# Performance work log

Measured on AMD Instinct MI355X. Metric: run time of the kernel, lower is better.

Reference implementation:

```python
import jax, jax.numpy as jnp
import numpy as np

U = 200000      # unique nodes
B = 20000       # node_list batch size
K = 33          # n_nbr_samples + self
F = 256         # feature_dim
E = 128         # emb_dim
BN_EPS = 1e-5


def setup_inputs() -> dict:
    key = jax.random.key(0)
    k1, k2, k3, k4 = jax.random.split(key, 4)
    return {
        "features": jax.random.normal(k1, (U, F), dtype=jnp.float32),
        "W": jax.random.normal(k2, (F, E), dtype=jnp.float32) * 0.05,
        "b": jax.random.normal(k3, (E,), dtype=jnp.float32) * 0.01,
        "gamma": jnp.ones((E,), dtype=jnp.float32),
        "beta": jnp.zeros((E,), dtype=jnp.float32),
        "sample_idx": jax.random.randint(k4, (B, K), 0, U, dtype=jnp.int64)
        if jax.config.jax_enable_x64 else jax.random.randint(k4, (B, K), 0, U, dtype=jnp.int32),
    }


def reference(features, W, b, gamma, beta, sample_idx):
    # fc: Linear -> BatchNorm1d (training-mode batch stats) -> Tanh; Dropout in eval (identity)
    h = features @ W + b                       # [U, E]
    mu = jnp.mean(h, axis=0)                   # [E]
    var = jnp.var(h, axis=0)                   # biased var, as torch BN uses for normalization
    h = jnp.tanh(gamma * (h - mu) * jax.lax.rsqrt(var + BN_EPS) + beta)  # [U, E]
    # Row-normalized 0/1 mask matmul == mean over the K distinct sampled unique-node rows
    gathered = h[sample_idx]                   # [B, K, E] irregular gather
    return jnp.mean(gathered, axis=1)          # [B, E]
```

## Files before the change

kernel.cpp:

```cpp
#include <hip/hip_runtime.h>

#define U_NODES 200000
#define B_ROWS  20000
#define K_S     33
#define F_DIM   256
#define E_DIM   128

typedef __bf16 bf16x8 __attribute__((ext_vector_type(8)));
typedef float  f32x4  __attribute__((ext_vector_type(4)));
typedef unsigned short ushortx4 __attribute__((ext_vector_type(4)));
typedef unsigned short ushortx8 __attribute__((ext_vector_type(8)));

__device__ __forceinline__ unsigned short f2bf(float f) {
    unsigned int u = __builtin_bit_cast(unsigned int, f);
    u += 0x7fffu + ((u >> 16) & 1u);
    return (unsigned short)(u >> 16);
}
__device__ __forceinline__ float bf2f(unsigned short s) {
    return __builtin_bit_cast(float, ((unsigned int)s) << 16);
}

__global__ void wprep_kernel(const float* __restrict__ W, unsigned short* __restrict__ Wt) {
    int n = blockIdx.x;
    int k = threadIdx.x;
    Wt[n * F_DIM + k] = f2bf(W[(size_t)k * E_DIM + n]);
}

__global__ __launch_bounds__(256) void gemm_stats_kernel(
    const float* __restrict__ A, const unsigned short* __restrict__ Wt,
    unsigned short* __restrict__ h, float* __restrict__ gsum, float* __restrict__ gsq)
{
    __shared__ __attribute__((aligned(16))) char smem[32768];
    char* As = smem;
    char* Ws = smem + 16384;

    const int t    = threadIdx.x;
    const int lane = t & 63;
    const int wv   = t >> 6;
    const int m    = lane & 15;
    const int qd   = lane >> 4;
    const int row0 = blockIdx.x * 128;

    f32x4 acc0[8], acc1[8];
    #pragma unroll
    for (int ct = 0; ct < 8; ++ct) {
        acc0[ct] = (f32x4){0.f, 0.f, 0.f, 0.f};
        acc1[ct] = (f32x4){0.f, 0.f, 0.f, 0.f};
    }

    for (int kk = 0; kk < F_DIM; kk += 64) {
        #pragma unroll
        for (int i = 0; i < 8; ++i) {
            int flat = t + 256 * i;
            int r  = flat >> 4;
            int c4 = (flat & 15) * 4;
            int gr = row0 + r; if (gr >= U_NODES) gr = U_NODES - 1;
            float4 v = *(const float4*)(A + (size_t)gr * F_DIM + kk + c4);
            int q = c4 >> 3, half = (c4 >> 2) & 1;
            ushortx4 w4 = { f2bf(v.x), f2bf(v.y), f2bf(v.z), f2bf(v.w) };
            *(ushortx4*)(As + r * 128 + ((q ^ (r & 7)) << 4) + half * 8) = w4;
        }
        #pragma unroll
        for (int i = 0; i < 4; ++i) {
            int flat = t + 256 * i;
            int r = flat >> 3, q = flat & 7;
            ushortx8 v = *(const ushortx8*)(Wt + (size_t)r * F_DIM + kk + q * 8);
            *(ushortx8*)(Ws + r * 128 + ((q ^ (r & 7)) << 4)) = v;
        }
        __syncthreads();
        #pragma unroll
        for (int ks = 0; ks < 2; ++ks) {
            int q = ks * 4 + qd;
            int r0 = wv * 32 + m;
            int r1 = r0 + 16;
            bf16x8 a0 = *(const bf16x8*)(As + r0 * 128 + ((q ^ (r0 & 7)) << 4));
            bf16x8 a1 = *(const bf16x8*)(As + r1 * 128 + ((q ^ (r1 & 7)) << 4));
            #pragma unroll
            for (int ct = 0; ct < 8; ++ct) {
                int rb = ct * 16 + m;
                bf16x8 b = *(const bf16x8*)(Ws + rb * 128 + ((q ^ (rb & 7)) << 4));
                acc0[ct] = __builtin_amdgcn_mfma_f32_16x16x32_bf16(a0, b, acc0[ct], 0, 0, 0);
                acc1[ct] = __builtin_amdgcn_mfma_f32_16x16x32_bf16(a1, b, acc1[ct], 0, 0, 0);
            }
        }
        __syncthreads();
    }

    const bool full = (row0 + 128) <= U_NODES;
    float s[8], sq[8];
    #pragma unroll
    for (int ct = 0; ct < 8; ++ct) {
        float ss = 0.f, qq = 0.f;
        #pragma unroll
        for (int v = 0; v < 4; ++v) {
            float x0 = acc0[ct][v];
            float x1 = acc1[ct][v];
            if (full || (row0 + wv * 32 + qd * 4 + v) < U_NODES)      { ss += x0; qq += x0 * x0; }
            if (full || (row0 + wv * 32 + 16 + qd * 4 + v) < U_NODES) { ss += x1; qq += x1 * x1; }
        }
        s[ct] = ss; sq[ct] = qq;
    }
    float* red = (float*)smem;
    int rq = wv * 4 + qd;
    #pragma unroll
    for (int ct = 0; ct < 8; ++ct) red[rq * 128 + ct * 16 + m] = s[ct];
    __syncthreads();
    if (t < 128) {
        float tot = 0.f;
        #pragma unroll
        for (int i = 0; i < 16; ++i) tot += red[i * 128 + t];
        atomicAdd(&gsum[t], tot);
    }
    __syncthreads();
    #pragma unroll
    for (int ct = 0; ct < 8; ++ct) red[rq * 128 + ct * 16 + m] = sq[ct];
    __syncthreads();
    if (t < 128) {
        float tot = 0.f;
        #pragma unroll
        for (int i = 0; i < 16; ++i) tot += red[i * 128 + t];
        atomicAdd(&gsq[t], tot);
    }
    __syncthreads();

    unsigned short* tb = (unsigned short*)(smem + wv * 8192);
    #pragma unroll
    for (int ct = 0; ct < 8; ++ct)
        #pragma unroll
        for (int v = 0; v < 4; ++v) {
            tb[(qd * 4 + v) * 128 + ct * 16 + m]        = f2bf(acc0[ct][v]);
            tb[(16 + qd * 4 + v) * 128 + ct * 16 + m]   = f2bf(acc1[ct][v]);
        }
    __syncthreads();
    #pragma unroll
    for (int i = 0; i < 8; ++i) {
        int idx = lane + 64 * i;
        int r = idx >> 4, c8 = (idx & 15) * 8;
        int gr = row0 + wv * 32 + r;
        if (gr < U_NODES)
            *(ushortx8*)(h + (size_t)gr * E_DIM + c8) = *(const ushortx8*)(tb + r * 128 + c8);
    }
}

__global__ void finalize_kernel(const float* __restrict__ gsum, const float* __restrict__ gsq,
                                const float* __restrict__ gamma, const float* __restrict__ beta,
                                float* __restrict__ scale, float* __restrict__ shift)
{
    int e = threadIdx.x;
    float mu  = gsum[e] * (1.f / U_NODES);
    float var = gsq[e] * (1.f / U_NODES) - mu * mu;
    float inv = rsqrtf(var + 1e-5f);
    float sc  = gamma[e] * inv;
    scale[e] = sc;
    shift[e] = beta[e] - sc * mu;
}

__global__ __launch_bounds__(256) void gather_kernel(
    const unsigned short* __restrict__ h, const int* __restrict__ sidx_g,
    const float* __restrict__ scale, const float* __restrict__ shift,
    float* __restrict__ out)
{
    __shared__ int sl[16 * K_S];
    const int t  = threadIdx.x;
    const int g  = t & 15;
    const int r  = t >> 4;
    const int b0 = blockIdx.x * 16;
    for (int i = t; i < 16 * K_S; i += 256) sl[i] = sidx_g[(size_t)b0 * K_S + i];
    float scv[8], shv[8];
    *(float4*)&scv[0] = *(const float4*)(scale + g * 8);
    *(float4*)&scv[4] = *(const float4*)(scale + g * 8 + 4);
    *(float4*)&shv[0] = *(const float4*)(shift + g * 8);
    *(float4*)&shv[4] = *(const float4*)(shift + g * 8 + 4);
    __syncthreads();

    float acc[8] = {0.f, 0.f, 0.f, 0.f, 0.f, 0.f, 0.f, 0.f};
    #pragma unroll
    for (int k = 0; k < K_S; ++k) {
        int idx = sl[r * K_S + k];
        ushortx8 v = *(const ushortx8*)(h + (size_t)idx * E_DIM + g * 8);
        #pragma unroll
        for (int j = 0; j < 8; ++j) {
            float x  = bf2f(v[j]) * scv[j] + shv[j];
            float ex = __expf(2.f * x);
            acc[j] += 1.f - 2.f * __builtin_amdgcn_rcpf(ex + 1.f);
        }
    }
    float* op = out + (size_t)(b0 + r) * E_DIM + g * 8;
    *(float4*)(op)     = make_float4(acc[0] * (1.f / K_S), acc[1] * (1.f / K_S),
                                     acc[2] * (1.f / K_S), acc[3] * (1.f / K_S));
    *(float4*)(op + 4) = make_float4(acc[4] * (1.f / K_S), acc[5] * (1.f / K_S),
                                     acc[6] * (1.f / K_S), acc[7] * (1.f / K_S));
}

extern "C" void kernel_launch(void* const* d_in, const int* in_sizes, int n_in,
                              void* d_out, int out_size, void* d_ws, size_t ws_size,
                              hipStream_t stream) {
    const float* features = (const float*)d_in[0];
    const float* W        = (const float*)d_in[1];
    const float* gamma    = (const float*)d_in[3];
    const float* beta     = (const float*)d_in[4];
    const int*   sample   = (const int*)d_in[5];
    float* out = (float*)d_out;

    float* gsum  = (float*)d_ws;
    float* gsq   = gsum + 128;
    float* scale = gsq + 128;
    float* shift = scale + 128;
    unsigned short* Wt = (unsigned short*)(shift + 128);
    unsigned short* h  = Wt + 128 * 256;

    hipMemsetAsync(gsum, 0, 2 * 128 * sizeof(float), stream);
    wprep_kernel<<<128, 256, 0, stream>>>(W, Wt);
    gemm_stats_kernel<<<(U_NODES + 127) / 128, 256, 0, stream>>>(features, Wt, h, gsum, gsq);
    finalize_kernel<<<1, 128, 0, stream>>>(gsum, gsq, gamma, beta, scale, shift);
    gather_kernel<<<B_ROWS / 16, 256, 0, stream>>>(h, sample, scale, shift, out);
}
```

Baseline: 343.4 us.

## Load A fragments directly to registers with double-buffered prefetch; stage full W once

The GEMM no longer stages the feature tile through LDS. Each lane loads its own A fragment from global memory into registers, converts it to bf16 in registers, and double-buffers the loads so the next K-chunk is fetched while MFMAs run on the current one. All of W (256x128 bf16) is staged into LDS once, which removes the per-chunk barriers, and the sum and sum-of-squares reductions now share one pass. The cost is a 64KB LDS allocation, which may limit occupancy, plus more registers and less coalesced global reads of A.

```diff
diff --git a/kernel.cpp b/kernel.cpp
--- a/kernel.cpp
+++ b/kernel.cpp
@@ -19,6 +19,12 @@
 __device__ __forceinline__ float bf2f(unsigned short s) {
     return __builtin_bit_cast(float, ((unsigned int)s) << 16);
 }
+__device__ __forceinline__ bf16x8 pack_bf8(f32x4 a, f32x4 b) {
+    ushortx8 r;
+    r[0] = f2bf(a[0]); r[1] = f2bf(a[1]); r[2] = f2bf(a[2]); r[3] = f2bf(a[3]);
+    r[4] = f2bf(b[0]); r[5] = f2bf(b[1]); r[6] = f2bf(b[2]); r[7] = f2bf(b[3]);
+    return __builtin_bit_cast(bf16x8, r);
+}
 
 __global__ void wprep_kernel(const float* __restrict__ W, unsigned short* __restrict__ Wt) {
     int n = blockIdx.x;
@@ -30,9 +36,8 @@
     const float* __restrict__ A, const unsigned short* __restrict__ Wt,
     unsigned short* __restrict__ h, float* __restrict__ gsum, float* __restrict__ gsq)
 {
-    __shared__ __attribute__((aligned(16))) char smem[32768];
-    char* As = smem;
-    char* Ws = smem + 16384;
+    __shared__ __attribute__((aligned(16))) char smem[65536];
+    char* Ws = smem;
 
     const int t    = threadIdx.x;
     const int lane = t & 63;
@@ -41,6 +46,52 @@
     const int qd   = lane >> 4;
     const int row0 = blockIdx.x * 128;
 
+    int gr0 = row0 + wv * 32 + m;       if (gr0 >= U_NODES) gr0 = U_NODES - 1;
+    int gr1 = row0 + wv * 32 + 16 + m;  if (gr1 >= U_NODES) gr1 = U_NODES - 1;
+    const float* pa0 = A + (size_t)gr0 * F_DIM + qd * 8;
+    const float* pa1 = A + (size_t)gr1 * F_DIM + qd * 8;
+
+#define LOAD_CHUNK(P, c) do {                                                  \
+        P[0] = *(const f32x4*)(pa0 + (c) * 64);                                \
+        P[1] = *(const f32x4*)(pa0 + (c) * 64 + 4);                            \
+        P[2] = *(const f32x4*)(pa0 + (c) * 64 + 32);                           \
+        P[3] = *(const f32x4*)(pa0 + (c) * 64 + 36);                           \
+        P[4] = *(const f32x4*)(pa1 + (c) * 64);                                \
+        P[5] = *(const f32x4*)(pa1 + (c) * 64 + 4);                            \
+        P[6] = *(const f32x4*)(pa1 + (c) * 64 + 32);                           \
+        P[7] = *(const f32x4*)(pa1 + (c) * 64 + 36);                           \
+    } while (0)
+
+#define COMPUTE_CHUNK(P, c) do {                                               \
+        bf16x8 a00 = pack_bf8(P[0], P[1]);                                     \
+        bf16x8 a01 = pack_bf8(P[2], P[3]);                                     \
+        bf16x8 a10 = pack_bf8(P[4], P[5]);                                     \
+        bf16x8 a11 = pack_bf8(P[6], P[7]);                                     \
+        _Pragma("unroll")                                                      \
+        for (int ct = 0; ct < 8; ++ct) {                                       \
+            int rb = ct * 16 + m;                                              \
+            bf16x8 b0 = *(const bf16x8*)(Ws + rb * 512 +                       \
+                            ((((c) * 8 + qd) ^ (rb & 7)) << 4));               \
+            acc0[ct] = __builtin_amdgcn_mfma_f32_16x16x32_bf16(a00, b0, acc0[ct], 0, 0, 0); \
+            acc1[ct] = __builtin_amdgcn_mfma_f32_16x16x32_bf16(a10, b0, acc1[ct], 0, 0, 0); \
+            bf16x8 b1 = *(const bf16x8*)(Ws + rb * 512 +                       \
+                            ((((c) * 8 + 4 + qd) ^ (rb & 7)) << 4));           \
+            acc0[ct] = __builtin_amdgcn_mfma_f32_16x16x32_bf16(a01, b1, acc0[ct], 0, 0, 0); \
+            acc1[ct] = __builtin_amdgcn_mfma_f32_16x16x32_bf16(a11, b1, acc1[ct], 0, 0, 0); \
+        }                                                                      \
+    } while (0)
+
+    f32x4 p0[8], p1[8];
+    LOAD_CHUNK(p0, 0);
+
+    #pragma unroll
+    for (int i = 0; i < 16; ++i) {
+        int flat = t + 256 * i;
+        int r = flat >> 5, q = flat & 31;
+        ushortx8 v = *(const ushortx8*)(Wt + (size_t)r * F_DIM + q * 8);
+        *(ushortx8*)(Ws + r * 512 + ((q ^ (r & 7)) << 4)) = v;
+    }
+
     f32x4 acc0[8], acc1[8];
     #pragma unroll
     for (int ct = 0; ct < 8; ++ct) {
@@ -48,43 +99,20 @@
         acc1[ct] = (f32x4){0.f, 0.f, 0.f, 0.f};
     }
 
-    for (int kk = 0; kk < F_DIM; kk += 64) {
-        #pragma unroll
-        for (int i = 0; i < 8; ++i) {
-            int flat = t + 256 * i;
-            int r  = flat >> 4;
-            int c4 = (flat & 15) * 4;
-            int gr = row0 + r; if (gr >= U_NODES) gr = U_NODES - 1;
-            float4 v = *(const float4*)(A + (size_t)gr * F_DIM + kk + c4);
-            int q = c4 >> 3, half = (c4 >> 2) & 1;
-            ushortx4 w4 = { f2bf(v.x), f2bf(v.y), f2bf(v.z), f2bf(v.w) };
-            *(ushortx4*)(As + r * 128 + ((q ^ (r & 7)) << 4) + half * 8) = w4;
-        }
-        #pragma unroll
-        for (int i = 0; i < 4; ++i) {
-            int flat = t + 256 * i;
-            int r = flat >> 3, q = flat & 7;
-            ushortx8 v = *(const ushortx8*)(Wt + (size_t)r * F_DIM + kk + q * 8);
-            *(ushortx8*)(Ws + r * 128 + ((q ^ (r & 7)) << 4)) = v;
-        }
-        __syncthreads();
-        #pragma unroll
-        for (int ks = 0; ks < 2; ++ks) {
-            int q = ks * 4 + qd;
-            int r0 = wv * 32 + m;
-            int r1 = r0 + 16;
-            bf16x8 a0 = *(const bf16x8*)(As + r0 * 128 + ((q ^ (r0 & 7)) << 4));
-            bf16x8 a1 = *(const bf16x8*)(As + r1 * 128 + ((q ^ (r1 & 7)) << 4));
-            #pragma unroll
-            for (int ct = 0; ct < 8; ++ct) {
-                int rb = ct * 16 + m;
-                bf16x8 b = *(const bf16x8*)(Ws + rb * 128 + ((q ^ (rb & 7)) << 4));
-                acc0[ct] = __builtin_amdgcn_mfma_f32_16x16x32_bf16(a0, b, acc0[ct], 0, 0, 0);
-                acc1[ct] = __builtin_amdgcn_mfma_f32_16x16x32_bf16(a1, b, acc1[ct], 0, 0, 0);
-            }
-        }
-        __syncthreads();
-    }
+    __syncthreads();
+
+    LOAD_CHUNK(p1, 1);
+    COMPUTE_CHUNK(p0, 0);
+    LOAD_CHUNK(p0, 2);
+    COMPUTE_CHUNK(p1, 1);
+    LOAD_CHUNK(p1, 3);
+    COMPUTE_CHUNK(p0, 2);
+    COMPUTE_CHUNK(p1, 3);
+
+#undef LOAD_CHUNK
+#undef COMPUTE_CHUNK
+
+    __syncthreads();
 
     const bool full = (row0 + 128) <= U_NODES;
     float s[8], sq[8];
@@ -100,26 +128,26 @@
         }
         s[ct] = ss; sq[ct] = qq;
     }
-    float* red = (float*)smem;
+    float* redS = (float*)smem;
+    float* redQ = (float*)(smem + 8192);
     int rq = wv * 4 + qd;
     #pragma unroll
-    for (int ct = 0; ct < 8; ++ct) red[rq * 128 + ct * 16 + m] = s[ct];
+    for (int ct = 0; ct < 8; ++ct) {
+        redS[rq * 128 + ct * 16 + m] = s[ct];
+        redQ[rq * 128 + ct * 16 + m] = sq[ct];
+    }
     __syncthreads();
     if (t < 128) {
         float tot = 0.f;
         #pragma unroll
-        for (int i = 0; i < 16; ++i) tot += red[i * 128 + t];
+        for (int i = 0; i < 16; ++i) tot += redS[i * 128 + t];
         atomicAdd(&gsum[t], tot);
-    }
-    __syncthreads();
-    #pragma unroll
-    for (int ct = 0; ct < 8; ++ct) red[rq * 128 + ct * 16 + m] = sq[ct];
-    __syncthreads();
-    if (t < 128) {
+    } else {
+        int e = t - 128;
         float tot = 0.f;
         #pragma unroll
-        for (int i = 0; i < 16; ++i) tot += red[i * 128 + t];
-        atomicAdd(&gsq[t], tot);
+        for (int i = 0; i < 16; ++i) tot += redQ[i * 128 + e];
+        atomicAdd(&gsq[e], tot);
     }
     __syncthreads();
 
```

After: 346.1 us. About the same (+0.8%).
